# Optimization experiments

Measured on AMD Instinct MI355X. Metric: run time of the kernel, lower is better.

## Reference

```python
import jax, jax.numpy as jnp
import numpy as np

D_MODEL = 1024
HEADS = 16
DK = D_MODEL // HEADS  # 64
B, S = 1, 4096


def setup_inputs() -> dict:
    key = jax.random.key(0)
    ks = jax.random.split(key, 11)
    sd = 1.0 / np.sqrt(D_MODEL)
    return {
        "q": jax.random.normal(ks[0], (B, S, D_MODEL), jnp.float32),
        "k": jax.random.normal(ks[1], (B, S, D_MODEL), jnp.float32),
        "v": jax.random.normal(ks[2], (B, S, D_MODEL), jnp.float32),
        "Wq": jax.random.uniform(ks[3], (D_MODEL, D_MODEL), jnp.float32, -sd, sd),
        "bq": jax.random.uniform(ks[4], (D_MODEL,), jnp.float32, -sd, sd),
        "Wk": jax.random.uniform(ks[5], (D_MODEL, DK), jnp.float32, -sd, sd),
        "bk": jax.random.uniform(ks[6], (DK,), jnp.float32, -sd, sd),
        "Wv": jax.random.uniform(ks[7], (D_MODEL, DK), jnp.float32, -sd, sd),
        "bv": jax.random.uniform(ks[8], (DK,), jnp.float32, -sd, sd),
        "Wo": jax.random.uniform(ks[9], (D_MODEL, D_MODEL), jnp.float32, -sd, sd),
        "bo": jax.random.uniform(ks[10], (D_MODEL,), jnp.float32, -sd, sd),
    }


def reference(q, k, v, Wq, bq, Wk, bk, Wv, bv, Wo, bo):
    b, s, d = q.shape
    # projections: q -> [b, H, s, dk]; k, v -> single shared head [b, s, dk]
    qp = (q @ Wq + bq).reshape(b, s, HEADS, DK).transpose(0, 2, 1, 3)
    kp = k @ Wk + bk  # [b, s, dk]
    vp = v @ Wv + bv  # [b, s, dk]
    # NOTE: original module never applies self.scale or dropout — faithful.
    scores = jnp.einsum('bhqd,bkd->bhqk', qp, kp)  # [b, H, s, s]
    attn = jax.nn.softmax(scores, axis=-1)
    out = jnp.einsum('bhqk,bkd->bhqd', attn, vp)  # [b, H, s, dk]
    out = out.transpose(0, 2, 1, 3).reshape(b, s, d)
    return out @ Wo + bo
```

## Files before the change

### kernel.cpp

```cpp
#include <hip/hip_runtime.h>
#include <hip/hip_bf16.h>
#include <stdint.h>

typedef __bf16 bf16_t;
typedef __attribute__((ext_vector_type(8))) __bf16 bf16x8;
typedef __attribute__((ext_vector_type(4))) __bf16 bf16x4;
typedef __attribute__((ext_vector_type(4))) float f32x4;

#define S_LEN 4096
#define DMODEL 1024
#define NHEADS 16
#define DKH 64

__device__ __forceinline__ f32x4 mfma16(bf16x8 a, bf16x8 b, f32x4 c) {
  return __builtin_amdgcn_mfma_f32_16x16x32_bf16(a, b, c, 0, 0, 0);
}

template <typename TS>
__device__ __forceinline__ bf16x8 load8_bf16(const TS* g) {
  bf16x8 o;
  if constexpr (sizeof(TS) == 4) {
    const float4 f0 = *(const float4*)(g);
    const float4 f1 = *(const float4*)(g + 4);
    o[0] = (bf16_t)f0.x; o[1] = (bf16_t)f0.y; o[2] = (bf16_t)f0.z; o[3] = (bf16_t)f0.w;
    o[4] = (bf16_t)f1.x; o[5] = (bf16_t)f1.y; o[6] = (bf16_t)f1.z; o[7] = (bf16_t)f1.w;
  } else {
    o = *(const bf16x8*)(g);
  }
  return o;
}

template <typename TS>
__device__ __forceinline__ void stage_tile64(const TS* __restrict__ g, int gstride,
                                             bf16_t* lds, int rows, int tid) {
  for (int i = tid; i < rows * 8; i += 256) {
    const int row = i >> 3, j = i & 7;
    const int c = j ^ (row & 7);
    bf16x8 v = load8_bf16(g + (size_t)row * gstride + j * 8);
    *(bf16x8*)((char*)lds + row * 128 + c * 16) = v;
  }
}

__device__ __forceinline__ bf16x8 frag64(const bf16_t* lds, int row, int g) {
  return *(const bf16x8*)((const char*)lds + row * 128 + ((g ^ (row & 7)) * 16));
}

__device__ __forceinline__ void gload16(const bf16_t* g, bf16_t* lds) {
  __builtin_amdgcn_global_load_lds(
      (const __attribute__((address_space(1))) unsigned int*)g,
      (__attribute__((address_space(3))) unsigned int*)lds, 16, 0, 0);
}

__global__ __launch_bounds__(256) void convert_bf16(const float* __restrict__ src,
                                                    bf16_t* __restrict__ dst) {
  const size_t i = (size_t)(blockIdx.x * 256 + threadIdx.x) * 8;
  bf16x8 v = load8_bf16(src + i);
  *(bf16x8*)(dst + i) = v;
}

__global__ __launch_bounds__(256) void prep_weights(const float* __restrict__ Wq,
                                                    const float* __restrict__ Wo,
                                                    const float* __restrict__ Wk,
                                                    const float* __restrict__ Wv,
                                                    bf16_t* __restrict__ Wqt,
                                                    bf16_t* __restrict__ Wot,
                                                    bf16_t* __restrict__ Wkt,
                                                    bf16_t* __restrict__ Wvt) {
  const int b = blockIdx.x;
  const float* src; bf16_t* dst; int ss, ds_, bx, by;
  if (b < 256)      { src = Wq; dst = Wqt; ss = 1024; ds_ = 1024; bx = b & 15;         by = b >> 4; }
  else if (b < 512) { src = Wo; dst = Wot; ss = 1024; ds_ = 1024; bx = (b - 256) & 15; by = (b - 256) >> 4; }
  else if (b < 528) { src = Wk; dst = Wkt; ss = 64;   ds_ = 1024; bx = 0;              by = b - 512; }
  else              { src = Wv; dst = Wvt; ss = 64;   ds_ = 1024; bx = 0;              by = b - 528; }

  __shared__ bf16_t t[64][65];
  const int tid = threadIdx.x;
  const int r0 = by * 64, c0 = bx * 64;
#pragma unroll
  for (int it = 0; it < 2; ++it) {
    int idx = tid + it * 256;
    int r = idx >> 3, c8 = idx & 7;
    bf16x8 v = load8_bf16(src + (size_t)(r0 + r) * ss + c0 + c8 * 8);
#pragma unroll
    for (int j = 0; j < 8; ++j) t[c8 * 8 + j][r] = v[j];
  }
  __syncthreads();
#pragma unroll
  for (int it = 0; it < 2; ++it) {
    int idx = tid + it * 256;
    int r = idx >> 3, c8 = idx & 7;
    bf16x8 v;
#pragma unroll
    for (int j = 0; j < 8; ++j) v[j] = t[r][c8 * 8 + j];
    *(bf16x8*)(dst + (size_t)(c0 + r) * ds_ + r0 + c8 * 8) = v;
  }
}

template <typename TC>
__global__ __launch_bounds__(256) void gemm_nt_dma(const bf16_t* __restrict__ A, int lda,
                                                   const bf16_t* __restrict__ Bt, int ldb,
                                                   const float* __restrict__ bias,
                                                   TC* __restrict__ C, int ldc, int K) {
  constexpr int BM = 128, BN = 64;
  __shared__ __align__(16) bf16_t As[2][BM * 64];
  __shared__ __align__(16) bf16_t Bs[2][BN * 64];
  const int tid = threadIdx.x, l = tid & 63, w = tid >> 6;
  const int lr = l & 15, quad = l >> 4;
  const int m0 = blockIdx.y * BM, n0 = blockIdx.x * BN;
  const int wm = w * 32;

  const int srow = l >> 3;
  const int sch = (l & 7) ^ srow;
  const bf16_t* a0 = A + (size_t)(m0 + w * 32 + srow) * lda + sch * 8;
  const bf16_t* b0 = Bt + (size_t)(n0 + w * 16 + srow) * ldb + sch * 8;

  f32x4 zero = {0.f, 0.f, 0.f, 0.f};
  f32x4 acc[2][4];
#pragma unroll
  for (int i = 0; i < 2; ++i)
#pragma unroll
    for (int j = 0; j < 4; ++j) acc[i][j] = zero;

  const int nt = K >> 6;

#pragma unroll
  for (int sub = 0; sub < 4; ++sub)
    gload16(a0 + (size_t)sub * 8 * lda, &As[0][(w * 32 + sub * 8) * 64]);
#pragma unroll
  for (int sub = 0; sub < 2; ++sub)
    gload16(b0 + (size_t)sub * 8 * ldb, &Bs[0][(w * 16 + sub * 8) * 64]);
  asm volatile("s_waitcnt vmcnt(0)" ::: "memory");
  __builtin_amdgcn_s_barrier();
  asm volatile("" ::: "memory");

  for (int t = 0; t < nt; ++t) {
    const int cur = t & 1;
    if (t + 1 < nt) {
#pragma unroll
      for (int sub = 0; sub < 4; ++sub)
        gload16(a0 + (size_t)(t + 1) * 64 + (size_t)sub * 8 * lda,
                &As[cur ^ 1][(w * 32 + sub * 8) * 64]);
#pragma unroll
      for (int sub = 0; sub < 2; ++sub)
        gload16(b0 + (size_t)(t + 1) * 64 + (size_t)sub * 8 * ldb,
                &Bs[cur ^ 1][(w * 16 + sub * 8) * 64]);
    }
    const bf16_t* Ac = &As[cur][0];
    const bf16_t* Bc = &Bs[cur][0];
#pragma unroll
    for (int kc = 0; kc < 2; ++kc) {
      bf16x8 af[2], bfr[4];
#pragma unroll
      for (int rt = 0; rt < 2; ++rt) af[rt] = frag64(Ac, wm + rt * 16 + lr, kc * 4 + quad);
#pragma unroll
      for (int ct = 0; ct < 4; ++ct) bfr[ct] = frag64(Bc, ct * 16 + lr, kc * 4 + quad);
#pragma unroll
      for (int rt = 0; rt < 2; ++rt)
#pragma unroll
        for (int ct = 0; ct < 4; ++ct) acc[rt][ct] = mfma16(af[rt], bfr[ct], acc[rt][ct]);
    }
    asm volatile("s_waitcnt vmcnt(0) lgkmcnt(0)" ::: "memory");
    __builtin_amdgcn_s_barrier();
    asm volatile("" ::: "memory");
  }

#pragma unroll
  for (int rt = 0; rt < 2; ++rt)
#pragma unroll
    for (int ct = 0; ct < 4; ++ct) {
      const int n = n0 + ct * 16 + lr;
      const float bv = bias[n];
      const int mb = m0 + wm + rt * 16 + quad * 4;
#pragma unroll
      for (int r = 0; r < 4; ++r)
        C[(size_t)(mb + r) * ldc + n] = (TC)(acc[rt][ct][r] + bv);
    }
}

template <int KSPLIT>
__global__ __launch_bounds__(256) void gemm_projkv_partial(const float* __restrict__ Ak,
                                                           const float* __restrict__ Av,
                                                           const bf16_t* __restrict__ Wkt,
                                                           const bf16_t* __restrict__ Wvt,
                                                           float* __restrict__ Pk,
                                                           float* __restrict__ Pv) {
  const float* A = blockIdx.z ? Av : Ak;
  const bf16_t* Bt = blockIdx.z ? Wvt : Wkt;
  float* part = blockIdx.z ? Pv : Pk;

  __shared__ __align__(16) bf16_t As[128 * 64];
  __shared__ __align__(16) bf16_t Bs[64 * 64];
  const int tid = threadIdx.x, l = tid & 63, w = tid >> 6;
  const int lr = l & 15, quad = l >> 4;
  const int kp = blockIdx.x, m0 = blockIdx.y * 128;
  const int kBase = kp * (DMODEL / KSPLIT);
  const int wm = w * 32;

  f32x4 zero = {0.f, 0.f, 0.f, 0.f};
  f32x4 acc[2][4];
#pragma unroll
  for (int i = 0; i < 2; ++i)
#pragma unroll
    for (int j = 0; j < 4; ++j) acc[i][j] = zero;

  for (int t = 0; t < (DMODEL / KSPLIT) / 64; ++t) {
    __syncthreads();
    stage_tile64(A + (size_t)m0 * DMODEL + kBase + t * 64, DMODEL, As, 128, tid);
    stage_tile64(Bt + kBase + t * 64, DMODEL, Bs, 64, tid);
    __syncthreads();
#pragma unroll
    for (int kc = 0; kc < 2; ++kc) {
      bf16x8 af[2], bfr[4];
#pragma unroll
      for (int rt = 0; rt < 2; ++rt) af[rt] = frag64(As, wm + rt * 16 + lr, kc * 4 + quad);
#pragma unroll
      for (int ct = 0; ct < 4; ++ct) bfr[ct] = frag64(Bs, ct * 16 + lr, kc * 4 + quad);
#pragma unroll
      for (int rt = 0; rt < 2; ++rt)
#pragma unroll
        for (int ct = 0; ct < 4; ++ct) acc[rt][ct] = mfma16(af[rt], bfr[ct], acc[rt][ct]);
    }
  }
#pragma unroll
  for (int rt = 0; rt < 2; ++rt)
#pragma unroll
    for (int ct = 0; ct < 4; ++ct) {
      const int n = ct * 16 + lr;
      const int mb = m0 + wm + rt * 16 + quad * 4;
#pragma unroll
      for (int r = 0; r < 4; ++r)
        part[(size_t)kp * S_LEN * 64 + (size_t)(mb + r) * 64 + n] = acc[rt][ct][r];
    }
}

__global__ __launch_bounds__(256) void reduce_kv(const float* __restrict__ Pk,
                                                 const float* __restrict__ Pv,
                                                 const float* __restrict__ bk,
                                                 const float* __restrict__ bv,
                                                 bf16_t* __restrict__ kvb,
                                                 bf16_t* __restrict__ vtb) {
  const int gid = blockIdx.x * 256 + threadIdx.x;
  const int s = gid >> 6, d = gid & 63;
  float sk = bk[d], sv = bv[d];
#pragma unroll
  for (int p = 0; p < 8; ++p) {
    sk += Pk[(size_t)p * S_LEN * 64 + gid];
    sv += Pv[(size_t)p * S_LEN * 64 + gid];
  }
  kvb[(size_t)s * 128 + d] = (bf16_t)sk;
  kvb[(size_t)s * 128 + 64 + d] = (bf16_t)sv;
  vtb[(size_t)d * S_LEN + s] = (bf16_t)sv;
}

__global__ __launch_bounds__(512, 4) void mqa_attn(const bf16_t* __restrict__ qp,
                                                   const bf16_t* __restrict__ kvb,
                                                   const bf16_t* __restrict__ vtb,
                                                   bf16_t* __restrict__ outp) {
  __shared__ __align__(16) bf16_t Ks[2][64 * 64];
  __shared__ __align__(16) bf16_t Vs[2][64 * 64];
  __shared__ __align__(16) bf16_t Ps[8][16 * 64];
  const int tid = threadIdx.x, l = tid & 63, w = tid >> 6;
  const int lr = l & 15, quad = l >> 4;
  const int h = blockIdx.y;
  const int q0 = blockIdx.x * 128;
  const int qrow = q0 + w * 16 + lr;
  char* Pw = (char*)&Ps[w][0];

  const int srow = w * 8 + (l >> 3);
  const int schunk = (l & 7) ^ (srow & 7);
  const bf16_t* ksrc = kvb + (size_t)srow * 128 + schunk * 8;
  const bf16_t* vsrc = vtb + (size_t)srow * S_LEN + schunk * 8;

  const bf16x8 qf0 = *(const bf16x8*)(qp + (size_t)qrow * DMODEL + h * DKH + quad * 8);
  const bf16x8 qf1 = *(const bf16x8*)(qp + (size_t)qrow * DMODEL + h * DKH + 32 + quad * 8);

  f32x4 zero = {0.f, 0.f, 0.f, 0.f};
  f32x4 o[4];
#pragma unroll
  for (int dt = 0; dt < 4; ++dt) o[dt] = zero;
  float li = 0.f;

  gload16(ksrc, &Ks[0][w * 512]);
  gload16(vsrc, &Vs[0][w * 512]);
  asm volatile("s_waitcnt vmcnt(0)" ::: "memory");
  __builtin_amdgcn_s_barrier();
  asm volatile("" ::: "memory");

  for (int t = 0; t < S_LEN / 64; ++t) {
    const int cur = t & 1;
    if (t + 1 < S_LEN / 64) {
      gload16(ksrc + (size_t)(t + 1) * 8192, &Ks[cur ^ 1][w * 512]);
      gload16(vsrc + (size_t)(t + 1) * 64, &Vs[cur ^ 1][w * 512]);
    }
    const bf16_t* Kc = &Ks[cur][0];
    const bf16_t* Vc = &Vs[cur][0];

    f32x4 st[4];
#pragma unroll
    for (int kt = 0; kt < 4; ++kt) {
      const bf16x8 kf0 = frag64(Kc, kt * 16 + lr, quad);
      const bf16x8 kf1 = frag64(Kc, kt * 16 + lr, 4 + quad);
      f32x4 a = zero;
      a = mfma16(kf0, qf0, a);
      a = mfma16(kf1, qf1, a);
      st[kt] = a;
    }

    float rs = 0.f;
#pragma unroll
    for (int kt = 0; kt < 4; ++kt) {
      bf16x4 pk;
#pragma unroll
      for (int r = 0; r < 4; ++r) {
        const float p = __expf(st[kt][r]);
        rs += p;
        pk[r] = (bf16_t)p;
      }
      *(bf16x4*)(Pw + lr * 128 + (((kt * 4 + quad) ^ ((lr & 7) << 1)) << 3)) = pk;
    }
    li += rs;
    asm volatile("s_waitcnt lgkmcnt(0)" ::: "memory");

#pragma unroll
    for (int kc2 = 0; kc2 < 2; ++kc2) {
      const bf16x8 pf = *(const bf16x8*)(Pw + lr * 128 + (((kc2 * 4 + quad) ^ (lr & 7)) << 4));
#pragma unroll
      for (int dt = 0; dt < 4; ++dt) {
        const bf16x8 vf = frag64(Vc, dt * 16 + lr, kc2 * 4 + quad);
        o[dt] = mfma16(vf, pf, o[dt]);
      }
    }

    asm volatile("s_waitcnt vmcnt(0) lgkmcnt(0)" ::: "memory");
    __builtin_amdgcn_s_barrier();
    asm volatile("" ::: "memory");
  }

  li += __shfl_xor(li, 16, 64);
  li += __shfl_xor(li, 32, 64);
  const float inv = 1.f / li;
#pragma unroll
  for (int dt = 0; dt < 4; ++dt) {
    bf16x4 ov;
#pragma unroll
    for (int rg = 0; rg < 4; ++rg) ov[rg] = (bf16_t)(o[dt][rg] * inv);
    *(bf16x4*)(outp + (size_t)qrow * DMODEL + h * DKH + dt * 16 + quad * 4) = ov;
  }
}

extern "C" void kernel_launch(void* const* d_in, const int* in_sizes, int n_in,
                              void* d_out, int out_size, void* d_ws, size_t ws_size,
                              hipStream_t stream) {
  const float* q  = (const float*)d_in[0];
  const float* k  = (const float*)d_in[1];
  const float* v  = (const float*)d_in[2];
  const float* Wq = (const float*)d_in[3];
  const float* bq = (const float*)d_in[4];
  const float* Wk = (const float*)d_in[5];
  const float* bk = (const float*)d_in[6];
  const float* Wv = (const float*)d_in[7];
  const float* bv = (const float*)d_in[8];
  const float* Wo = (const float*)d_in[9];
  const float* bo = (const float*)d_in[10];
  float* out = (float*)d_out;
  char* ws = (char*)d_ws;

  const size_t MB = 1u << 20;
  bf16_t* Wqt = (bf16_t*)(ws);
  bf16_t* Wot = (bf16_t*)(ws + 2 * MB);
  bf16_t* Wkt = (bf16_t*)(ws + 4 * MB);
  bf16_t* Wvt = (bf16_t*)(ws + 4 * MB + 131072);
  bf16_t* kvb = (bf16_t*)(ws + 4 * MB + 524288);
  bf16_t* vtb = (bf16_t*)(ws + 5 * MB + 524288);
  float*  Pk   = (float*)(ws + 6 * MB);
  float*  Pv   = (float*)(ws + 14 * MB);
  bf16_t* qb   = (bf16_t*)(ws + 6 * MB);
  bf16_t* qp   = (bf16_t*)(ws + 14 * MB);
  bf16_t* attn = (bf16_t*)(ws + 6 * MB);

  dim3 B(256);
  prep_weights<<<dim3(544), B, 0, stream>>>(Wq, Wo, Wk, Wv, Wqt, Wot, Wkt, Wvt);

  gemm_projkv_partial<8><<<dim3(8, 32, 2), B, 0, stream>>>(k, v, Wkt, Wvt, Pk, Pv);
  reduce_kv<<<dim3(1024), B, 0, stream>>>(Pk, Pv, bk, bv, kvb, vtb);

  convert_bf16<<<dim3(2048), B, 0, stream>>>(q, qb);
  gemm_nt_dma<bf16_t><<<dim3(16, 32), B, 0, stream>>>(qb, 1024, Wqt, 1024, bq, qp, 1024, 1024);

  mqa_attn<<<dim3(32, 16), dim3(512), 0, stream>>>(qp, kvb, vtb, attn);

  gemm_nt_dma<float><<<dim3(16, 32), B, 0, stream>>>(attn, 1024, Wot, 1024, bo, out, 1024, 1024);
}
```

Before: 247.2 us.

## Process two query tiles per wave in MQA attention, halving block size

The attention kernel now runs 4 waves per block instead of 8. Each wave handles 32 query rows as two 16-row sub-tiles that share the K and V fragments read from LDS. This halves LDS fragment reads per MFMA and gives each wave more independent MFMA chains, at the cost of doubled accumulator registers and fewer waves to hide the per-tile barriers. Each wave now issues twice as many K/V tile loads per iteration.

```diff
diff --git a/kernel.cpp b/kernel.cpp
--- a/kernel.cpp
+++ b/kernel.cpp
@@ -252,36 +252,45 @@
   vtb[(size_t)d * S_LEN + s] = (bf16_t)sv;
 }
 
-__global__ __launch_bounds__(512, 4) void mqa_attn(const bf16_t* __restrict__ qp,
+__global__ __launch_bounds__(256, 3) void mqa_attn(const bf16_t* __restrict__ qp,
                                                    const bf16_t* __restrict__ kvb,
                                                    const bf16_t* __restrict__ vtb,
                                                    bf16_t* __restrict__ outp) {
   __shared__ __align__(16) bf16_t Ks[2][64 * 64];
   __shared__ __align__(16) bf16_t Vs[2][64 * 64];
-  __shared__ __align__(16) bf16_t Ps[8][16 * 64];
+  __shared__ __align__(16) bf16_t Ps[4][2][16 * 64];
   const int tid = threadIdx.x, l = tid & 63, w = tid >> 6;
   const int lr = l & 15, quad = l >> 4;
   const int h = blockIdx.y;
   const int q0 = blockIdx.x * 128;
-  const int qrow = q0 + w * 16 + lr;
-  char* Pw = (char*)&Ps[w][0];
-
-  const int srow = w * 8 + (l >> 3);
-  const int schunk = (l & 7) ^ (srow & 7);
-  const bf16_t* ksrc = kvb + (size_t)srow * 128 + schunk * 8;
-  const bf16_t* vsrc = vtb + (size_t)srow * S_LEN + schunk * 8;
-
-  const bf16x8 qf0 = *(const bf16x8*)(qp + (size_t)qrow * DMODEL + h * DKH + quad * 8);
-  const bf16x8 qf1 = *(const bf16x8*)(qp + (size_t)qrow * DMODEL + h * DKH + 32 + quad * 8);
+  const int qrA = q0 + w * 32 + lr;
+  const int qrB = qrA + 16;
+  char* Pw0 = (char*)&Ps[w][0][0];
+  char* Pw1 = (char*)&Ps[w][1][0];
+
+  const int srow8 = l >> 3;
+  const int sch = (l & 7) ^ srow8;
+  const int wr = w * 16;
+  const bf16_t* ksrc = kvb + (size_t)(wr + srow8) * 128 + sch * 8;
+  const bf16_t* vsrc = vtb + (size_t)(wr + srow8) * S_LEN + sch * 8;
+
+  const bf16_t* qbase = qp + (size_t)qrA * DMODEL + h * DKH;
+  const bf16x8 qfA0 = *(const bf16x8*)(qbase + quad * 8);
+  const bf16x8 qfA1 = *(const bf16x8*)(qbase + 32 + quad * 8);
+  const bf16_t* qbase2 = qp + (size_t)qrB * DMODEL + h * DKH;
+  const bf16x8 qfB0 = *(const bf16x8*)(qbase2 + quad * 8);
+  const bf16x8 qfB1 = *(const bf16x8*)(qbase2 + 32 + quad * 8);
 
   f32x4 zero = {0.f, 0.f, 0.f, 0.f};
-  f32x4 o[4];
-#pragma unroll
-  for (int dt = 0; dt < 4; ++dt) o[dt] = zero;
-  float li = 0.f;
-
-  gload16(ksrc, &Ks[0][w * 512]);
-  gload16(vsrc, &Vs[0][w * 512]);
+  f32x4 o0[4], o1[4];
+#pragma unroll
+  for (int dt = 0; dt < 4; ++dt) { o0[dt] = zero; o1[dt] = zero; }
+  float li0 = 0.f, li1 = 0.f;
+
+  gload16(ksrc, &Ks[0][wr * 64]);
+  gload16(ksrc + 1024, &Ks[0][(wr + 8) * 64]);
+  gload16(vsrc, &Vs[0][wr * 64]);
+  gload16(vsrc + (size_t)8 * S_LEN, &Vs[0][(wr + 8) * 64]);
   asm volatile("s_waitcnt vmcnt(0)" ::: "memory");
   __builtin_amdgcn_s_barrier();
   asm volatile("" ::: "memory");
@@ -289,45 +298,58 @@
   for (int t = 0; t < S_LEN / 64; ++t) {
     const int cur = t & 1;
     if (t + 1 < S_LEN / 64) {
-      gload16(ksrc + (size_t)(t + 1) * 8192, &Ks[cur ^ 1][w * 512]);
-      gload16(vsrc + (size_t)(t + 1) * 64, &Vs[cur ^ 1][w * 512]);
+      gload16(ksrc + (size_t)(t + 1) * 8192, &Ks[cur ^ 1][wr * 64]);
+      gload16(ksrc + (size_t)(t + 1) * 8192 + 1024, &Ks[cur ^ 1][(wr + 8) * 64]);
+      gload16(vsrc + (size_t)(t + 1) * 64, &Vs[cur ^ 1][wr * 64]);
+      gload16(vsrc + (size_t)(t + 1) * 64 + (size_t)8 * S_LEN, &Vs[cur ^ 1][(wr + 8) * 64]);
     }
     const bf16_t* Kc = &Ks[cur][0];
     const bf16_t* Vc = &Vs[cur][0];
 
-    f32x4 st[4];
+    f32x4 st0[4], st1[4];
 #pragma unroll
     for (int kt = 0; kt < 4; ++kt) {
       const bf16x8 kf0 = frag64(Kc, kt * 16 + lr, quad);
       const bf16x8 kf1 = frag64(Kc, kt * 16 + lr, 4 + quad);
-      f32x4 a = zero;
-      a = mfma16(kf0, qf0, a);
-      a = mfma16(kf1, qf1, a);
-      st[kt] = a;
-    }
-
-    float rs = 0.f;
+      f32x4 a0 = mfma16(kf0, qfA0, zero);
+      a0 = mfma16(kf1, qfA1, a0);
+      st0[kt] = a0;
+      f32x4 a1 = mfma16(kf0, qfB0, zero);
+      a1 = mfma16(kf1, qfB1, a1);
+      st1[kt] = a1;
+    }
+
+    float rs0 = 0.f, rs1 = 0.f;
 #pragma unroll
     for (int kt = 0; kt < 4; ++kt) {
-      bf16x4 pk;
+      bf16x4 p0, p1;
 #pragma unroll
       for (int r = 0; r < 4; ++r) {
-        const float p = __expf(st[kt][r]);
-        rs += p;
-        pk[r] = (bf16_t)p;
+        const float e0 = __expf(st0[kt][r]);
+        rs0 += e0;
+        p0[r] = (bf16_t)e0;
+        const float e1 = __expf(st1[kt][r]);
+        rs1 += e1;
+        p1[r] = (bf16_t)e1;
       }
-      *(bf16x4*)(Pw + lr * 128 + (((kt * 4 + quad) ^ ((lr & 7) << 1)) << 3)) = pk;
-    }
-    li += rs;
+      const int poff = ((kt * 4 + quad) ^ ((lr & 7) << 1)) << 3;
+      *(bf16x4*)(Pw0 + lr * 128 + poff) = p0;
+      *(bf16x4*)(Pw1 + lr * 128 + poff) = p1;
+    }
+    li0 += rs0;
+    li1 += rs1;
     asm volatile("s_waitcnt lgkmcnt(0)" ::: "memory");
 
 #pragma unroll
     for (int kc2 = 0; kc2 < 2; ++kc2) {
-      const bf16x8 pf = *(const bf16x8*)(Pw + lr * 128 + (((kc2 * 4 + quad) ^ (lr & 7)) << 4));
+      const int poff = ((kc2 * 4 + quad) ^ (lr & 7)) << 4;
+      const bf16x8 pf0 = *(const bf16x8*)(Pw0 + lr * 128 + poff);
+      const bf16x8 pf1 = *(const bf16x8*)(Pw1 + lr * 128 + poff);
 #pragma unroll
       for (int dt = 0; dt < 4; ++dt) {
         const bf16x8 vf = frag64(Vc, dt * 16 + lr, kc2 * 4 + quad);
-        o[dt] = mfma16(vf, pf, o[dt]);
+        o0[dt] = mfma16(vf, pf0, o0[dt]);
+        o1[dt] = mfma16(vf, pf1, o1[dt]);
       }
     }
 
@@ -336,15 +358,22 @@
     asm volatile("" ::: "memory");
   }
 
-  li += __shfl_xor(li, 16, 64);
-  li += __shfl_xor(li, 32, 64);
-  const float inv = 1.f / li;
+  li0 += __shfl_xor(li0, 16, 64);
+  li0 += __shfl_xor(li0, 32, 64);
+  li1 += __shfl_xor(li1, 16, 64);
+  li1 += __shfl_xor(li1, 32, 64);
+  const float inv0 = 1.f / li0;
+  const float inv1 = 1.f / li1;
 #pragma unroll
   for (int dt = 0; dt < 4; ++dt) {
-    bf16x4 ov;
-#pragma unroll
-    for (int rg = 0; rg < 4; ++rg) ov[rg] = (bf16_t)(o[dt][rg] * inv);
-    *(bf16x4*)(outp + (size_t)qrow * DMODEL + h * DKH + dt * 16 + quad * 4) = ov;
+    bf16x4 ovA, ovB;
+#pragma unroll
+    for (int rg = 0; rg < 4; ++rg) {
+      ovA[rg] = (bf16_t)(o0[dt][rg] * inv0);
+      ovB[rg] = (bf16_t)(o1[dt][rg] * inv1);
+    }
+    *(bf16x4*)(outp + (size_t)qrA * DMODEL + h * DKH + dt * 16 + quad * 4) = ovA;
+    *(bf16x4*)(outp + (size_t)qrB * DMODEL + h * DKH + dt * 16 + quad * 4) = ovB;
   }
 }
 
@@ -387,7 +416,7 @@
   convert_bf16<<<dim3(2048), B, 0, stream>>>(q, qb);
   gemm_nt_dma<bf16_t><<<dim3(16, 32), B, 0, stream>>>(qb, 1024, Wqt, 1024, bq, qp, 1024, 1024);
 
-  mqa_attn<<<dim3(32, 16), dim3(512), 0, stream>>>(qp, kvb, vtb, attn);
+  mqa_attn<<<dim3(32, 16), B, 0, stream>>>(qp, kvb, vtb, attn);
 
   gemm_nt_dma<float><<<dim3(16, 32), B, 0, stream>>>(attn, 1024, Wot, 1024, bo, out, 1024, 1024);
 }
```

Measured after the change: 261.9 us. 5.9% more time.
